# Performance work log

Measured on AMD Instinct MI355X. Metric: run time of the kernel, lower is better.

## Reference

```python
import jax, jax.numpy as jnp
import numpy as np

B, S, H, L, HEADS, VOCAB, POS = 32, 240, 1024, 8, 16, 48, 240
D = H // HEADS


def setup_inputs() -> dict:
    key = jax.random.key(0)
    ks = jax.random.split(key, 20)
    p = lambda k, shape: jax.random.normal(k, shape, jnp.float32) * 0.02
    x = jax.random.normal(ks[0], (B, S, VOCAB), jnp.float32)
    lengths = jnp.sort(jax.random.randint(ks[1], (B,), 120, S + 1))[::-1]
    lengths = lengths.at[0].set(S)  # padded max length == S
    return {
        "x": x,
        "w_emb": p(ks[2], (VOCAB, H)),
        "p_emb": p(ks[3], (POS, H)),
        "Wq": p(ks[4], (L, H, H)), "bq": p(ks[5], (L, H)),
        "Wk": p(ks[6], (L, H, H)), "bk": p(ks[7], (L, H)),
        "Wv": p(ks[8], (L, H, H)), "bv": p(ks[9], (L, H)),
        "W1": p(ks[10], (L, H, H)), "b1": p(ks[11], (L, H)),
        "W2": p(ks[12], (L, H, H)), "b2": p(ks[13], (L, H)),
        "ln1_s": jnp.ones((L, H), jnp.float32), "ln1_b": jnp.zeros((L, H), jnp.float32),
        "ln2_s": jnp.ones((L, H), jnp.float32), "ln2_b": jnp.zeros((L, H), jnp.float32),
        "Wfc": p(ks[14], (H, 4)), "bfc": p(ks[15], (4,)),
        "lengths": lengths,
    }


def _ln(x, s, b):
    m = jnp.mean(x, -1, keepdims=True)
    v = jnp.mean((x - m) ** 2, -1, keepdims=True)
    return (x - m) / jnp.sqrt(v + 1e-5) * s + b


def reference(x, w_emb, p_emb, Wq, bq, Wk, bk, Wv, bv, W1, b1, W2, b2,
              ln1_s, ln1_b, ln2_s, ln2_b, Wfc, bfc, lengths):
    tokens = jnp.argmax(x, -1)                      # [B,S] argmax over feature dim (48)
    valid = jnp.arange(S)[None, :] < lengths[:, None]  # [B,S] query-row validity
    # pack/unpack zeros out embeddings at padded positions; pos-enc added everywhere
    z = w_emb[tokens] * valid[..., None].astype(jnp.float32) + p_emb[None, :S]
    causal = jnp.tril(jnp.ones((S, S), bool))
    scale = 1.0 / jnp.sqrt(jnp.float32(H))          # source divides by sqrt(hidden), not sqrt(d_head)
    for i in range(L):
        q = (z @ Wq[i] + bq[i]).reshape(B, S, HEADS, D)
        k = (z @ Wk[i] + bk[i]).reshape(B, S, HEADS, D)
        v = (z @ Wv[i] + bv[i]).reshape(B, S, HEADS, D)
        scores = jnp.einsum('bqhd,bkhd->bhqk', q, k) * scale
        scores = jnp.where(causal, scores, -jnp.inf)
        # softmax over causal keys; padded query rows are zeroed (torch NaN->0 path)
        atten = jax.nn.softmax(scores, -1) * valid[:, None, :, None].astype(jnp.float32)
        out = jnp.einsum('bhqk,bkhd->bqhd', atten, v).reshape(B, S, H)
        z1 = _ln(z + out, ln1_s[i], ln1_b[i])       # dropout off in eval
        ff = jax.nn.gelu(z1 @ W1[i] + b1[i], approximate=False) @ W2[i] + b2[i]
        z = _ln(z1 + ff, ln2_s[i], ln2_b[i])
    z2 = jnp.mean(z, axis=1)                        # mean-pool includes padded positions (faithful)
    return jax.nn.softmax(z2 @ Wfc + bfc, axis=-1)
```

## Files before the change

kernel.cpp:

```cpp
#include <hip/hip_runtime.h>
#include <hip/hip_bf16.h>

#define Bz 32
#define Sz 240
#define Hz 1024
#define Lz 8
#define NHEADS 16
#define NVOCAB 48
#define DHEAD 64
#define VT_STRIDE 264

typedef unsigned short u16;
typedef unsigned int u32;
typedef __attribute__((ext_vector_type(8))) short short8v;
typedef __attribute__((ext_vector_type(4))) float floatx4;

__device__ __forceinline__ int get_len(const int* __restrict__ L, int b) {
  return (L[1] == 0) ? L[2 * b] : L[b];
}
__device__ __forceinline__ u16 f2bf(float f) {
  u32 u = __float_as_uint(f);
  return (u16)((u + 0x7FFFu + ((u >> 16) & 1u)) >> 16);
}
__device__ __forceinline__ float bf2f(u16 s) {
  return __uint_as_float(((u32)s) << 16);
}
__device__ __forceinline__ void async_copy16(const u16* g, u16* l) {
  __builtin_amdgcn_global_load_lds(
      (const __attribute__((address_space(1))) u32*)g,
      (__attribute__((address_space(3))) u32*)l, 16, 0, 0);
}

__global__ __launch_bounds__(256) void embed_kernel(
    const float* __restrict__ x, const float* __restrict__ w_emb,
    const float* __restrict__ p_emb, const int* __restrict__ lengths,
    float* __restrict__ z, u16* __restrict__ z_bf) {
  int bs = blockIdx.x;
  int b = bs / Sz, s = bs % Sz;
  __shared__ int stok;
  if (threadIdx.x == 0) {
    const float* xr = x + (size_t)bs * NVOCAB;
    float best = xr[0]; int bi = 0;
    for (int j = 1; j < NVOCAB; ++j) {
      float v = xr[j];
      if (v > best) { best = v; bi = j; }
    }
    stok = bi;
  }
  __syncthreads();
  int tok = stok;
  float valid = (s < get_len(lengths, b)) ? 1.f : 0.f;
  const float* we = w_emb + (size_t)tok * Hz;
  const float* pe = p_emb + (size_t)s * Hz;
  size_t base = (size_t)bs * Hz;
  for (int h = threadIdx.x; h < Hz; h += blockDim.x) {
    float v = we[h] * valid + pe[h];
    z[base + h] = v;
    z_bf[base + h] = f2bf(v);
  }
}

__global__ __launch_bounds__(256) void bias_concat(
    const float* __restrict__ bq, const float* __restrict__ bk,
    const float* __restrict__ bv, float* __restrict__ dst) {
  int i = blockIdx.x * 256 + threadIdx.x;
  int l = i / 3072, c = i % 3072;
  float v = (c < 1024) ? bq[l * 1024 + c]
          : (c < 2048) ? bk[l * 1024 + c - 1024]
                       : bv[l * 1024 + c - 2048];
  dst[i] = v;
}

struct WconvArgs { const float* src[5]; u16* dst[5]; };
__global__ __launch_bounds__(256) void wconv5(WconvArgs a) {
  __shared__ u16 T[32][33];
  const float* W = a.src[blockIdx.z];
  u16* wt = a.dst[blockIdx.z];
  int bi = blockIdx.y, bj = blockIdx.x;
  int r = threadIdx.x >> 3, c4 = (threadIdx.x & 7) * 4;
  float4 w4 = *(const float4*)(W + (size_t)(bi * 32 + r) * Hz + bj * 32 + c4);
  T[r][c4 + 0] = f2bf(w4.x); T[r][c4 + 1] = f2bf(w4.y);
  T[r][c4 + 2] = f2bf(w4.z); T[r][c4 + 3] = f2bf(w4.w);
  __syncthreads();
  u32 lo = (u32)T[c4 + 0][r] | ((u32)T[c4 + 1][r] << 16);
  u32 hi = (u32)T[c4 + 2][r] | ((u32)T[c4 + 3][r] << 16);
  uint2 val; val.x = lo; val.y = hi;
  *(uint2*)(wt + (size_t)(bj * 32 + r) * Hz + bi * 32 + c4) = val;
}

template <int BN, bool OUTBF16, bool GELU, bool RESID>
__global__ __launch_bounds__(512, 2) void gemm_mfma(
    const u16* __restrict__ A, const u16* __restrict__ Wt,
    const float* __restrict__ bias, const float* __restrict__ resid,
    void* __restrict__ Cv, int nco) {
  constexpr int MT = (BN == 256) ? 8 : 4;
  constexpr int WGC = (BN == 256) ? 4 : 2;
  constexpr int BKT = BN * 32;
  __shared__ u16 As[2][16384];
  __shared__ u16 Bs[2][BN * 64];
  int tid = threadIdx.x;
  int nwg = (int)gridDim.x;
  int id0 = blockIdx.x;
  int id = (id0 & 7) * (nwg >> 3) + (id0 >> 3);
  int ncols = nco / BN;
  int row0 = (id / ncols) * 256;
  int col0 = (id % ncols) * BN;

  int w = tid >> 6, lane = tid & 63;
  int l15 = lane & 15, lq = lane >> 4;
  int wr = w / WGC, wc = w % WGC;
  floatx4 acc[MT][4] = {};

  const u16* gA0 = A + (size_t)(row0 + 32 * w + l15) * 1024 + 8 * lq;
  const u16* gA1 = gA0 + 16 * 1024;
  const u16* gB0 = Wt + (size_t)(col0 + (BN == 256 ? 32 : 16) * w + l15) * 1024 + 8 * lq;
  const u16* gB1 = gB0 + 16 * 1024;

  auto stage = [&](int bb, int kk) {
#pragma unroll
    for (int kt = 0; kt < 2; ++kt) {
      async_copy16(gA0 + kk + 32 * kt, &As[bb][kt * 8192 + (2 * w) * 512]);
      async_copy16(gA1 + kk + 32 * kt, &As[bb][kt * 8192 + (2 * w + 1) * 512]);
      if constexpr (BN == 256) {
        async_copy16(gB0 + kk + 32 * kt, &Bs[bb][kt * BKT + (2 * w) * 512]);
        async_copy16(gB1 + kk + 32 * kt, &Bs[bb][kt * BKT + (2 * w + 1) * 512]);
      } else {
        async_copy16(gB0 + kk + 32 * kt, &Bs[bb][kt * BKT + w * 512]);
      }
    }
  };

  int afrag_off[MT], bfrag_off[4];
#pragma unroll
  for (int i = 0; i < MT; ++i)
    afrag_off[i] = (wr * MT + i) * 512 + lq * 128 + l15 * 8;
#pragma unroll
  for (int j = 0; j < 4; ++j)
    bfrag_off[j] = (wc * 4 + j) * 512 + lq * 128 + l15 * 8;

  stage(0, 0);
  __syncthreads();
  int cur = 0;
  for (int k0 = 0; k0 < 1024; k0 += 64) {
    if (k0 + 64 < 1024) stage(cur ^ 1, k0 + 64);
#pragma unroll
    for (int kt = 0; kt < 2; ++kt) {
      short8v af[MT], bf[4];
#pragma unroll
      for (int i = 0; i < MT; ++i)
        af[i] = *(const short8v*)(&As[cur][kt * 8192 + afrag_off[i]]);
#pragma unroll
      for (int j = 0; j < 4; ++j)
        bf[j] = *(const short8v*)(&Bs[cur][kt * BKT + bfrag_off[j]]);
#pragma unroll
      for (int mi = 0; mi < MT; ++mi)
#pragma unroll
        for (int ni = 0; ni < 4; ++ni)
          acc[mi][ni] = __builtin_amdgcn_mfma_f32_16x16x32_bf16(
              af[mi], bf[ni], acc[mi][ni], 0, 0, 0);
    }
    __syncthreads();
    cur ^= 1;
  }

  int rowbase = row0 + wr * (MT * 16), colbase = col0 + wc * 64;
#pragma unroll
  for (int ni = 0; ni < 4; ++ni) {
    int col = colbase + ni * 16 + l15;
    float bcol = bias[col];
#pragma unroll
    for (int mi = 0; mi < MT; ++mi) {
      int rtop = rowbase + mi * 16 + lq * 4;
#pragma unroll
      for (int reg = 0; reg < 4; ++reg) {
        float vv = acc[mi][ni][reg] + bcol;
        if (RESID) vv += resid[(size_t)(rtop + reg) * nco + col];
        if (GELU) vv = 0.5f * vv * (1.f + erff(vv * 0.70710678118654752f));
        if (OUTBF16)
          ((u16*)Cv)[(size_t)(rtop + reg) * nco + col] = f2bf(vv);
        else
          ((float*)Cv)[(size_t)(rtop + reg) * nco + col] = vv;
      }
    }
  }
}

__global__ __launch_bounds__(256) void attention_kernel(
    const u16* __restrict__ qkv, const int* __restrict__ lengths,
    const float* __restrict__ zres, float* __restrict__ out) {
  const int LDQ = 3072;
  __shared__ u16 Vt[64 * VT_STRIDE];
  __shared__ u16 Pb[4][16 * 40];
  int hh = blockIdx.x & 1;
  int h = (blockIdx.x >> 1) & 15;
  int b = blockIdx.x >> 5;
  int tid = threadIdx.x;
  const size_t base = ((size_t)b * Sz) * LDQ + (size_t)h * DHEAD;
  const u16* qp = qkv + base;
  const u16* kp = qkv + base + 1024;
  const u16* vp = qkv + base + 2048;

  for (int idx = tid; idx < 256 * 16; idx += 256) {
    int key = idx >> 4, d4 = (idx & 15) * 4;
    uint2 vv;
    if (key < Sz) vv = *(const uint2*)(vp + (size_t)key * LDQ + d4);
    else { vv.x = 0u; vv.y = 0u; }
    Vt[(d4 + 0) * VT_STRIDE + key] = (u16)(vv.x & 0xFFFF);
    Vt[(d4 + 1) * VT_STRIDE + key] = (u16)(vv.x >> 16);
    Vt[(d4 + 2) * VT_STRIDE + key] = (u16)(vv.y & 0xFFFF);
    Vt[(d4 + 3) * VT_STRIDE + key] = (u16)(vv.y >> 16);
  }
  __syncthreads();

  int w = tid >> 6, lane = tid & 63;
  int qgroup = lane >> 4, qcol = lane & 15;
  int len_b = get_len(lengths, b);

  for (int qt = hh * 8 + w; qt < hh * 8 + 8 && qt < 15; qt += 4) {
    const u16* qrow = qp + (size_t)(qt * 16 + qcol) * LDQ;
    short8v aq0 = *(const short8v*)(qrow + qgroup * 8);
    short8v aq1 = *(const short8v*)(qrow + 32 + qgroup * 8);
    floatx4 o0 = {0.f, 0.f, 0.f, 0.f}, o1 = o0, o2 = o0, o3 = o0;
    float m_run[4] = {-1e30f, -1e30f, -1e30f, -1e30f};
    float l_run[4] = {0.f, 0.f, 0.f, 0.f};
    int nsteps = (qt + 2) >> 1;

    for (int st = 0; st < nsteps; ++st) {
      int t0 = 2 * st, t1 = 2 * st + 1;
      bool has1 = (t1 <= qt);
      floatx4 s0 = {0.f, 0.f, 0.f, 0.f};
      {
        const u16* kr = kp + (size_t)(t0 * 16 + qcol) * LDQ;
        short8v bk0 = *(const short8v*)(kr + qgroup * 8);
        short8v bk1 = *(const short8v*)(kr + 32 + qgroup * 8);
        s0 = __builtin_amdgcn_mfma_f32_16x16x32_bf16(aq0, bk0, s0, 0, 0, 0);
        s0 = __builtin_amdgcn_mfma_f32_16x16x32_bf16(aq1, bk1, s0, 0, 0, 0);
      }
      floatx4 s1 = {0.f, 0.f, 0.f, 0.f};
      if (has1) {
        const u16* kr = kp + (size_t)(t1 * 16 + qcol) * LDQ;
        short8v bk0 = *(const short8v*)(kr + qgroup * 8);
        short8v bk1 = *(const short8v*)(kr + 32 + qgroup * 8);
        s1 = __builtin_amdgcn_mfma_f32_16x16x32_bf16(aq0, bk0, s1, 0, 0, 0);
        s1 = __builtin_amdgcn_mfma_f32_16x16x32_bf16(aq1, bk1, s1, 0, 0, 0);
      }
      int kg0 = t0 * 16 + qcol, kg1 = t1 * 16 + qcol;
      float p0[4], p1[4];
#pragma unroll
      for (int rg = 0; rg < 4; ++rg) {
        int row_g = qt * 16 + qgroup * 4 + rg;
        float x0 = (kg0 <= row_g) ? s0[rg] * 0.03125f : -1e30f;
        float x1 = (has1 && kg1 <= row_g) ? s1[rg] * 0.03125f : -1e30f;
        float mx = fmaxf(x0, x1);
        mx = fmaxf(mx, __shfl_xor(mx, 1));
        mx = fmaxf(mx, __shfl_xor(mx, 2));
        mx = fmaxf(mx, __shfl_xor(mx, 4));
        mx = fmaxf(mx, __shfl_xor(mx, 8));
        float mnew = fmaxf(m_run[rg], mx);
        float alpha = __expf(m_run[rg] - mnew);
        float e0 = __expf(x0 - mnew);
        float e1 = __expf(x1 - mnew);
        float rs = e0 + e1;
        rs += __shfl_xor(rs, 1);
        rs += __shfl_xor(rs, 2);
        rs += __shfl_xor(rs, 4);
        rs += __shfl_xor(rs, 8);
        l_run[rg] = l_run[rg] * alpha + rs;
        m_run[rg] = mnew;
        o0[rg] *= alpha; o1[rg] *= alpha; o2[rg] *= alpha; o3[rg] *= alpha;
        p0[rg] = e0; p1[rg] = e1;
      }
#pragma unroll
      for (int rg = 0; rg < 4; ++rg) {
        int rl = qgroup * 4 + rg;
        Pb[w][rl * 40 + qcol] = f2bf(p0[rg]);
        Pb[w][rl * 40 + 16 + qcol] = f2bf(p1[rg]);
      }
      __asm__ volatile("s_waitcnt lgkmcnt(0)" ::: "memory");
      short8v pa = *(const short8v*)(&Pb[w][qcol * 40 + qgroup * 8]);
      int kb0 = st * 32 + qgroup * 8;
      short8v bv0 = *(const short8v*)(&Vt[(0 * 16 + qcol) * VT_STRIDE + kb0]);
      short8v bv1 = *(const short8v*)(&Vt[(1 * 16 + qcol) * VT_STRIDE + kb0]);
      short8v bv2 = *(const short8v*)(&Vt[(2 * 16 + qcol) * VT_STRIDE + kb0]);
      short8v bv3 = *(const short8v*)(&Vt[(3 * 16 + qcol) * VT_STRIDE + kb0]);
      o0 = __builtin_amdgcn_mfma_f32_16x16x32_bf16(pa, bv0, o0, 0, 0, 0);
      o1 = __builtin_amdgcn_mfma_f32_16x16x32_bf16(pa, bv1, o1, 0, 0, 0);
      o2 = __builtin_amdgcn_mfma_f32_16x16x32_bf16(pa, bv2, o2, 0, 0, 0);
      o3 = __builtin_amdgcn_mfma_f32_16x16x32_bf16(pa, bv3, o3, 0, 0, 0);
    }

#pragma unroll
    for (int rg = 0; rg < 4; ++rg) {
      int row_g = qt * 16 + qgroup * 4 + rg;
      float vmask = (row_g < len_b) ? (1.f / l_run[rg]) : 0.f;
      size_t ob = ((size_t)b * Sz + row_g) * Hz + (size_t)h * DHEAD + qcol;
      out[ob]      = zres[ob]      + o0[rg] * vmask;
      out[ob + 16] = zres[ob + 16] + o1[rg] * vmask;
      out[ob + 32] = zres[ob + 32] + o2[rg] * vmask;
      out[ob + 48] = zres[ob + 48] + o3[rg] * vmask;
    }
  }
}

__global__ __launch_bounds__(256) void add_ln_kernel(
    float* __restrict__ z, u16* __restrict__ z_bf, const float* __restrict__ r,
    const float* __restrict__ gamma, const float* __restrict__ beta) {
  int bs = blockIdx.x, tid = threadIdx.x;
  size_t base = (size_t)bs * Hz;
  __shared__ float sred[256];
  float4 v4 = *(const float4*)(r + base + tid * 4);
  float sum = v4.x + v4.y + v4.z + v4.w;
  sred[tid] = sum; __syncthreads();
  for (int off = 128; off > 0; off >>= 1) {
    if (tid < off) sred[tid] += sred[tid + off];
    __syncthreads();
  }
  float mean = sred[0] * (1.f / Hz); __syncthreads();
  float dx = v4.x - mean, dy = v4.y - mean, dz = v4.z - mean, dw = v4.w - mean;
  sred[tid] = dx * dx + dy * dy + dz * dz + dw * dw; __syncthreads();
  for (int off = 128; off > 0; off >>= 1) {
    if (tid < off) sred[tid] += sred[tid + off];
    __syncthreads();
  }
  float rstd = rsqrtf(sred[0] * (1.f / Hz) + 1e-5f);
  float4 g4 = *(const float4*)(gamma + tid * 4);
  float4 b4 = *(const float4*)(beta + tid * 4);
  float4 o;
  o.x = dx * rstd * g4.x + b4.x;
  o.y = dy * rstd * g4.y + b4.y;
  o.z = dz * rstd * g4.z + b4.z;
  o.w = dw * rstd * g4.w + b4.w;
  *(float4*)(z + base + tid * 4) = o;
  uint2 pk;
  pk.x = (u32)f2bf(o.x) | ((u32)f2bf(o.y) << 16);
  pk.y = (u32)f2bf(o.z) | ((u32)f2bf(o.w) << 16);
  *(uint2*)(z_bf + base + tid * 4) = pk;
}

__global__ __launch_bounds__(256) void pool1_kernel(
    const float* __restrict__ z, float* __restrict__ pooled) {
  int chunk = blockIdx.x, b = blockIdx.y, tid = threadIdx.x;
  int h = chunk * 128 + (tid & 127);
  int half = tid >> 7;
  __shared__ float sred[256];
  const float* zp = z + ((size_t)b * Sz + half * 120) * Hz + h;
  float s = 0.f;
  for (int i = 0; i < 120; ++i) s += zp[(size_t)i * Hz];
  sred[tid] = s; __syncthreads();
  if (tid < 128)
    pooled[(size_t)b * Hz + chunk * 128 + tid] =
        (sred[tid] + sred[tid + 128]) * (1.f / Sz);
}

__global__ __launch_bounds__(256) void pool2_kernel(
    const float* __restrict__ pooled, const float* __restrict__ Wfc,
    const float* __restrict__ bfc, float* __restrict__ out) {
  int b = blockIdx.x, tid = threadIdx.x;
  __shared__ float red[256][4];
  float acc[4] = {0.f, 0.f, 0.f, 0.f};
#pragma unroll
  for (int j = 0; j < 4; ++j) {
    int hh = tid * 4 + j;
    float z2 = pooled[(size_t)b * Hz + hh];
#pragma unroll
    for (int c = 0; c < 4; ++c) acc[c] += z2 * Wfc[hh * 4 + c];
  }
#pragma unroll
  for (int c = 0; c < 4; ++c) red[tid][c] = acc[c];
  __syncthreads();
  for (int off = 128; off > 0; off >>= 1) {
    if (tid < off)
#pragma unroll
      for (int c = 0; c < 4; ++c) red[tid][c] += red[tid + off][c];
    __syncthreads();
  }
  if (tid == 0) {
    float lg[4], m = -1e30f;
#pragma unroll
    for (int c = 0; c < 4; ++c) { lg[c] = red[0][c] + bfc[c]; m = fmaxf(m, lg[c]); }
    float s = 0.f;
#pragma unroll
    for (int c = 0; c < 4; ++c) { lg[c] = expf(lg[c] - m); s += lg[c]; }
    float inv = 1.f / s;
#pragma unroll
    for (int c = 0; c < 4; ++c) out[b * 4 + c] = lg[c] * inv;
  }
}

extern "C" void kernel_launch(void* const* d_in, const int* in_sizes, int n_in,
                              void* d_out, int out_size, void* d_ws, size_t ws_size,
                              hipStream_t stream) {
  const float* x     = (const float*)d_in[0];
  const float* w_emb = (const float*)d_in[1];
  const float* p_emb = (const float*)d_in[2];
  const float* Wq = (const float*)d_in[3];
  const float* bq = (const float*)d_in[4];
  const float* Wk = (const float*)d_in[5];
  const float* bk = (const float*)d_in[6];
  const float* Wv = (const float*)d_in[7];
  const float* bv = (const float*)d_in[8];
  const float* W1 = (const float*)d_in[9];
  const float* b1 = (const float*)d_in[10];
  const float* W2 = (const float*)d_in[11];
  const float* b2 = (const float*)d_in[12];
  const float* ln1s = (const float*)d_in[13];
  const float* ln1b = (const float*)d_in[14];
  const float* ln2s = (const float*)d_in[15];
  const float* ln2b = (const float*)d_in[16];
  const float* Wfc  = (const float*)d_in[17];
  const float* bfc  = (const float*)d_in[18];
  const int* lengths = (const int*)d_in[19];
  float* out = (float*)d_out;

  const size_t BSH = (size_t)Bz * Sz * Hz;
  float* z    = (float*)d_ws;
  float* ao   = z + BSH;
  u16* z_bf   = (u16*)(ao + BSH);
  u16* ffb    = z_bf + BSH;
  u16* qkv    = ffb + BSH;
  u16* wt     = qkv + 3 * BSH;
  float* bqkv = (float*)(wt + 5 * 1024 * 1024);
  float* pooled = bqkv + Lz * 3072;

  embed_kernel<<<Bz * Sz, 256, 0, stream>>>(x, w_emb, p_emb, lengths, z, z_bf);
  bias_concat<<<Lz * 3072 / 256, 256, 0, stream>>>(bq, bk, bv, bqkv);

  for (int i = 0; i < Lz; ++i) {
    size_t wo = (size_t)i * Hz * Hz, bo = (size_t)i * Hz;
    WconvArgs wa;
    wa.src[0] = Wq + wo; wa.src[1] = Wk + wo; wa.src[2] = Wv + wo;
    wa.src[3] = W1 + wo; wa.src[4] = W2 + wo;
    wa.dst[0] = wt;                     wa.dst[1] = wt + 1024 * 1024;
    wa.dst[2] = wt + 2 * 1024 * 1024;   wa.dst[3] = wt + 3 * 1024 * 1024;
    wa.dst[4] = wt + 4 * 1024 * 1024;
    wconv5<<<dim3(32, 32, 5), 256, 0, stream>>>(wa);

    gemm_mfma<256, true, false, false><<<30 * 12, 512, 0, stream>>>(
        z_bf, wt, bqkv + (size_t)i * 3072, nullptr, qkv, 3072);
    attention_kernel<<<Bz * NHEADS * 2, 256, 0, stream>>>(qkv, lengths, z, ao);
    add_ln_kernel<<<Bz * Sz, 256, 0, stream>>>(z, z_bf, ao, ln1s + bo, ln1b + bo);
    gemm_mfma<128, true, true, false><<<30 * 8, 512, 0, stream>>>(
        z_bf, wt + 3 * 1024 * 1024, b1 + bo, nullptr, ffb, 1024);
    gemm_mfma<128, false, false, true><<<30 * 8, 512, 0, stream>>>(
        ffb, wt + 4 * 1024 * 1024, b2 + bo, z, ao, 1024);
    add_ln_kernel<<<Bz * Sz, 256, 0, stream>>>(z, z_bf, ao, ln2s + bo, ln2b + bo);
  }
  pool1_kernel<<<dim3(8, Bz), 256, 0, stream>>>(z, pooled);
  pool2_kernel<<<Bz, 256, 0, stream>>>(pooled, Wfc, bfc, out);
}
```

Baseline: 2.279 ms.

## Deepen GEMM pipeline: prefetch two tiles ahead with fine-grained vmcnt waits

```diff
diff --git a/kernel.cpp b/kernel.cpp
--- a/kernel.cpp
+++ b/kernel.cpp
@@ -139,27 +139,58 @@
     bfrag_off[j] = (wc * 4 + j) * 512 + lq * 128 + l15 * 8;
 
   stage(0, 0);
-  __syncthreads();
+  stage(1, 64);
+  if constexpr (BN == 256)
+    __asm__ volatile("s_waitcnt vmcnt(8)" ::: "memory");
+  else
+    __asm__ volatile("s_waitcnt vmcnt(6)" ::: "memory");
+  __builtin_amdgcn_s_barrier();
+  __builtin_amdgcn_sched_barrier(0);
+
   int cur = 0;
   for (int k0 = 0; k0 < 1024; k0 += 64) {
-    if (k0 + 64 < 1024) stage(cur ^ 1, k0 + 64);
-#pragma unroll
-    for (int kt = 0; kt < 2; ++kt) {
-      short8v af[MT], bf[4];
-#pragma unroll
-      for (int i = 0; i < MT; ++i)
-        af[i] = *(const short8v*)(&As[cur][kt * 8192 + afrag_off[i]]);
-#pragma unroll
-      for (int j = 0; j < 4; ++j)
-        bf[j] = *(const short8v*)(&Bs[cur][kt * BKT + bfrag_off[j]]);
-#pragma unroll
-      for (int mi = 0; mi < MT; ++mi)
-#pragma unroll
-        for (int ni = 0; ni < 4; ++ni)
-          acc[mi][ni] = __builtin_amdgcn_mfma_f32_16x16x32_bf16(
-              af[mi], bf[ni], acc[mi][ni], 0, 0, 0);
-    }
-    __syncthreads();
+    short8v af0[MT], bf0[4], af1[MT], bf1[4];
+#pragma unroll
+    for (int i = 0; i < MT; ++i) {
+      af0[i] = *(const short8v*)(&As[cur][afrag_off[i]]);
+      af1[i] = *(const short8v*)(&As[cur][8192 + afrag_off[i]]);
+    }
+#pragma unroll
+    for (int j = 0; j < 4; ++j) {
+      bf0[j] = *(const short8v*)(&Bs[cur][bfrag_off[j]]);
+      bf1[j] = *(const short8v*)(&Bs[cur][BKT + bfrag_off[j]]);
+    }
+    __asm__ volatile("s_waitcnt lgkmcnt(0)" ::: "memory");
+    __builtin_amdgcn_sched_barrier(0);
+    __builtin_amdgcn_s_barrier();
+    __builtin_amdgcn_sched_barrier(0);
+    if (k0 + 128 < 1024) stage(cur, k0 + 128);
+    __builtin_amdgcn_s_setprio(1);
+#pragma unroll
+    for (int mi = 0; mi < MT; ++mi)
+#pragma unroll
+      for (int ni = 0; ni < 4; ++ni)
+        acc[mi][ni] = __builtin_amdgcn_mfma_f32_16x16x32_bf16(
+            af0[mi], bf0[ni], acc[mi][ni], 0, 0, 0);
+#pragma unroll
+    for (int mi = 0; mi < MT; ++mi)
+#pragma unroll
+      for (int ni = 0; ni < 4; ++ni)
+        acc[mi][ni] = __builtin_amdgcn_mfma_f32_16x16x32_bf16(
+            af1[mi], bf1[ni], acc[mi][ni], 0, 0, 0);
+    __builtin_amdgcn_s_setprio(0);
+    if (k0 + 64 < 1024) {
+      if (k0 + 128 < 1024) {
+        if constexpr (BN == 256)
+          __asm__ volatile("s_waitcnt vmcnt(8)" ::: "memory");
+        else
+          __asm__ volatile("s_waitcnt vmcnt(6)" ::: "memory");
+      } else {
+        __asm__ volatile("s_waitcnt vmcnt(0)" ::: "memory");
+      }
+      __builtin_amdgcn_s_barrier();
+      __builtin_amdgcn_sched_barrier(0);
+    }
     cur ^= 1;
   }
 
```

After: 2.170 ms. 4.8% less time.

## Split GEMM k-tile into halves with fine-grained vmcnt waits and priority

Applied to the files above, without the earlier changes.

```diff
diff --git a/kernel.cpp b/kernel.cpp
--- a/kernel.cpp
+++ b/kernel.cpp
@@ -95,7 +95,7 @@
     void* __restrict__ Cv, int nco) {
   constexpr int MT = (BN == 256) ? 8 : 4;
   constexpr int WGC = (BN == 256) ? 4 : 2;
-  constexpr int BKT = BN * 32;
+  constexpr int BS_KH = BN * 32;
   __shared__ u16 As[2][16384];
   __shared__ u16 Bs[2][BN * 64];
   int tid = threadIdx.x;
@@ -116,17 +116,14 @@
   const u16* gB0 = Wt + (size_t)(col0 + (BN == 256 ? 32 : 16) * w + l15) * 1024 + 8 * lq;
   const u16* gB1 = gB0 + 16 * 1024;
 
-  auto stage = [&](int bb, int kk) {
-#pragma unroll
-    for (int kt = 0; kt < 2; ++kt) {
-      async_copy16(gA0 + kk + 32 * kt, &As[bb][kt * 8192 + (2 * w) * 512]);
-      async_copy16(gA1 + kk + 32 * kt, &As[bb][kt * 8192 + (2 * w + 1) * 512]);
-      if constexpr (BN == 256) {
-        async_copy16(gB0 + kk + 32 * kt, &Bs[bb][kt * BKT + (2 * w) * 512]);
-        async_copy16(gB1 + kk + 32 * kt, &Bs[bb][kt * BKT + (2 * w + 1) * 512]);
-      } else {
-        async_copy16(gB0 + kk + 32 * kt, &Bs[bb][kt * BKT + w * 512]);
-      }
+  auto stage_h = [&](int bb, int kk, int kt) {
+    async_copy16(gA0 + kk + 32 * kt, &As[bb][kt * 8192 + (2 * w) * 512]);
+    async_copy16(gA1 + kk + 32 * kt, &As[bb][kt * 8192 + (2 * w + 1) * 512]);
+    if constexpr (BN == 256) {
+      async_copy16(gB0 + kk + 32 * kt, &Bs[bb][kt * BS_KH + (2 * w) * 512]);
+      async_copy16(gB1 + kk + 32 * kt, &Bs[bb][kt * BS_KH + (2 * w + 1) * 512]);
+    } else {
+      async_copy16(gB0 + kk + 32 * kt, &Bs[bb][kt * BS_KH + w * 512]);
     }
   };
 
@@ -138,30 +135,78 @@
   for (int j = 0; j < 4; ++j)
     bfrag_off[j] = (wc * 4 + j) * 512 + lq * 128 + l15 * 8;
 
-  stage(0, 0);
-  __syncthreads();
+#define WAIT_VM_H()                                                  \
+  do {                                                               \
+    if constexpr (BN == 256)                                         \
+      __asm__ volatile("s_waitcnt vmcnt(4)" ::: "memory");           \
+    else                                                             \
+      __asm__ volatile("s_waitcnt vmcnt(3)" ::: "memory");           \
+  } while (0)
+
+  stage_h(0, 0, 0);
+  stage_h(0, 0, 1);
+  WAIT_VM_H();
+  __builtin_amdgcn_s_barrier();
+  __builtin_amdgcn_sched_barrier(0);
+
   int cur = 0;
-  for (int k0 = 0; k0 < 1024; k0 += 64) {
-    if (k0 + 64 < 1024) stage(cur ^ 1, k0 + 64);
-#pragma unroll
-    for (int kt = 0; kt < 2; ++kt) {
-      short8v af[MT], bf[4];
-#pragma unroll
-      for (int i = 0; i < MT; ++i)
-        af[i] = *(const short8v*)(&As[cur][kt * 8192 + afrag_off[i]]);
-#pragma unroll
-      for (int j = 0; j < 4; ++j)
-        bf[j] = *(const short8v*)(&Bs[cur][kt * BKT + bfrag_off[j]]);
-#pragma unroll
-      for (int mi = 0; mi < MT; ++mi)
-#pragma unroll
-        for (int ni = 0; ni < 4; ++ni)
-          acc[mi][ni] = __builtin_amdgcn_mfma_f32_16x16x32_bf16(
-              af[mi], bf[ni], acc[mi][ni], 0, 0, 0);
-    }
-    __syncthreads();
+  for (int i = 0; i < 16; ++i) {
+    int kks = (i + 1) << 6;
+    bool st = (i < 15);
+    short8v af[MT], bf[4];
+
+#pragma unroll
+    for (int m = 0; m < MT; ++m)
+      af[m] = *(const short8v*)(&As[cur][afrag_off[m]]);
+#pragma unroll
+    for (int n = 0; n < 4; ++n)
+      bf[n] = *(const short8v*)(&Bs[cur][bfrag_off[n]]);
+    if (st) stage_h(cur ^ 1, kks, 0);
+    __builtin_amdgcn_s_barrier();
+    __asm__ volatile("s_waitcnt lgkmcnt(0)" ::: "memory");
+    __builtin_amdgcn_sched_barrier(0);
+    __builtin_amdgcn_s_setprio(1);
+#pragma unroll
+    for (int mi = 0; mi < MT; ++mi)
+#pragma unroll
+      for (int ni = 0; ni < 4; ++ni)
+        acc[mi][ni] = __builtin_amdgcn_mfma_f32_16x16x32_bf16(
+            af[mi], bf[ni], acc[mi][ni], 0, 0, 0);
+    __builtin_amdgcn_s_setprio(0);
+    if (st) {
+      WAIT_VM_H();
+    } else {
+      __asm__ volatile("s_waitcnt vmcnt(0)" ::: "memory");
+    }
+    __builtin_amdgcn_s_barrier();
+    __builtin_amdgcn_sched_barrier(0);
+
+#pragma unroll
+    for (int m = 0; m < MT; ++m)
+      af[m] = *(const short8v*)(&As[cur][8192 + afrag_off[m]]);
+#pragma unroll
+    for (int n = 0; n < 4; ++n)
+      bf[n] = *(const short8v*)(&Bs[cur][BS_KH + bfrag_off[n]]);
+    if (st) stage_h(cur ^ 1, kks, 1);
+    __builtin_amdgcn_s_barrier();
+    __asm__ volatile("s_waitcnt lgkmcnt(0)" ::: "memory");
+    __builtin_amdgcn_sched_barrier(0);
+    __builtin_amdgcn_s_setprio(1);
+#pragma unroll
+    for (int mi = 0; mi < MT; ++mi)
+#pragma unroll
+      for (int ni = 0; ni < 4; ++ni)
+        acc[mi][ni] = __builtin_amdgcn_mfma_f32_16x16x32_bf16(
+            af[mi], bf[ni], acc[mi][ni], 0, 0, 0);
+    __builtin_amdgcn_s_setprio(0);
+    if (st) {
+      WAIT_VM_H();
+      __builtin_amdgcn_s_barrier();
+      __builtin_amdgcn_sched_barrier(0);
+    }
     cur ^= 1;
   }
+#undef WAIT_VM_H
 
   int rowbase = row0 + wr * (MT * 16), colbase = col0 + wc * 64;
 #pragma unroll
```

Result: faster. 1.984 ms (-12.9%).
